# Kernel optimization log

Hardware: AMD Instinct MI355X
Metric: run time of the kernel (lower is better)

## Reference

```python
import jax, jax.numpy as jnp
import numpy as np

MARGIN = 0.2
PAIR_EPS = 1e-6   # torch pairwise_distance eps inside TripletMarginLoss
NORM_EPS = 1e-12  # F.normalize eps


def setup_inputs() -> dict:
    key = jax.random.key(0)
    k1, k2, k3 = jax.random.split(key, 3)
    bs, C, D = 64, 1024, 64
    inputs = jax.random.normal(k1, (bs, C, D), dtype=jnp.float32)
    label = jax.random.randint(k2, (bs, C, 1), 0, 2).astype(jnp.float32)
    prot = jax.random.normal(k3, (C, D), dtype=jnp.float32)
    prot = prot / jnp.linalg.norm(prot, axis=1, keepdims=True)
    return {"inputs": inputs, "label": label, "pos_prot": prot, "only_update": 0}


def reference(inputs, label, pos_prot, only_update):
    bs, C, D = inputs.shape
    # F.normalize(p=2, dim=1) per class slice == normalize over last dim of [bs,C,D]
    nrm = jnp.linalg.norm(inputs, axis=-1, keepdims=True)
    x = inputs / jnp.maximum(nrm, NORM_EPS)                      # [bs,C,D]

    # torch.cdist(x, prot): euclidean distances [bs, C(anchor cls), C(prot)]
    x2 = jnp.sum(x * x, axis=-1)                                 # [bs,C]
    p2 = jnp.sum(pos_prot * pos_prot, axis=-1)                   # [C]
    xp = jnp.einsum('bcd,kd->bck', x, pos_prot)                  # [bs,C,C]
    d2 = x2[:, :, None] + p2[None, None, :] - 2.0 * xp
    prot_dist = jnp.sqrt(jnp.maximum(d2, 0.0))                   # [bs,C,C]

    # hard negative: nearest prototype excluding the anchor's own class
    # (argsort + skip-self loop == masked argmin)
    eye = jnp.eye(C, dtype=bool)[None, :, :]
    neg_cls = jnp.argmin(jnp.where(eye, jnp.inf, prot_dist), axis=-1)  # [bs,C]

    positives = pos_prot[None, :, :]                             # [1,C,D] (broadcast of repeat)
    negatives = pos_prot[neg_cls]                                # [bs,C,D]

    # TripletMarginLoss(margin=0.2, p=2, reduction='none'), eps inside distance
    d_ap = jnp.linalg.norm(x - positives + PAIR_EPS, axis=-1)    # [bs,C]
    d_an = jnp.linalg.norm(x - negatives + PAIR_EPS, axis=-1)    # [bs,C]
    tri = jnp.maximum(d_ap - d_an + MARGIN, 0.0)                 # [bs,C]

    w = label[:, :, 0]                                           # [bs,C]
    loss = jnp.mean(jnp.sum(tri * w, axis=-1) / jnp.sum(w, axis=-1))
    return loss
```

## Files before the change

kernel.cpp:

```cpp
#include <hip/hip_runtime.h>
#include <cfloat>

#define BS 64
#define C  1024
#define D  64
#define CT 128
#define NX8 (BS * C * D / 8)

typedef __attribute__((ext_vector_type(8))) short short8;
typedef __attribute__((ext_vector_type(4))) float f32x4;
typedef unsigned short ushort_t;
typedef unsigned int uint_t;

__device__ __forceinline__ ushort_t f2bf(float f) {
    uint_t u = __float_as_uint(f);
    u += 0x7fffu + ((u >> 16) & 1u);
    return (ushort_t)(u >> 16);
}

__global__ __launch_bounds__(256)
void prep_cvt(const float* __restrict__ inputs, const float* __restrict__ prot,
              ushort_t* __restrict__ xhg, ushort_t* __restrict__ phg)
{
    const int idx = blockIdx.x * 256 + threadIdx.x;
    const bool isX = idx < NX8;
    const int rel = isX ? idx : idx - NX8;
    const float* sb = isX ? inputs : prot;
    ushort_t* db = isX ? xhg : phg;

    const int ft = rel >> 7, w = rel & 127, h = w >> 6, ln = w & 63;
    const int rr = ft * 16 + (ln & 15), dg = h * 4 + (ln >> 4);
    const float* s = sb + (size_t)rr * D + dg * 8;
    float4 a = *(const float4*)s;
    float4 b2 = *(const float4*)(s + 4);
    float x[8] = {a.x, a.y, a.z, a.w, b2.x, b2.y, b2.z, b2.w};
    short8 hv;
    #pragma unroll
    for (int e = 0; e < 8; e++) hv[e] = (short)f2bf(x[e]);
    ((short8*)db)[rel] = hv;
}

__global__ __launch_bounds__(512, 4)
void triplet_mfma(const float* __restrict__ inputs,
                  const float* __restrict__ label,
                  const float* __restrict__ prot,
                  const ushort_t* __restrict__ xhg,
                  const ushort_t* __restrict__ phg,
                  float* __restrict__ part)
{
    __shared__ short8 bsh[32 * 128];
    __shared__ uint_t redk[CT][4];
    __shared__ float  wred[16];

    const int tid  = threadIdx.x;
    const int lane = tid & 63;
    const int wid  = tid >> 6;
    const int wr   = wid >> 2;
    const int wc   = wid & 3;
    const int b    = blockIdx.x >> 3;
    const int c0   = (blockIdx.x & 7) * CT;

    const short8* BH = (const short8*)phg;
    const short8* XH = (const short8*)xhg;

    const size_t ftb = (size_t)blockIdx.x * 8 + wr * 4;
    short8 ah[4][2];
    #pragma unroll
    for (int i = 0; i < 4; i++) {
        ah[i][0] = XH[(ftb + i) * 128 + lane];
        ah[i][1] = XH[(ftb + i) * 128 + 64 + lane];
    }

    uint_t bestk[16];
    #pragma unroll
    for (int q = 0; q < 16; q++) bestk[q] = 0u;

    const uint_t MMASK = 0xFFFFFC00u;
    const int rowtile0 = (c0 >> 4) + wr * 4;
    const int rsub = (lane >> 4) * 4;
    const int csub = lane & 15;

    auto process = [&](int jg, short8 b0, short8 b1) {
        const uint_t cidx = (uint_t)(1023 - (jg * 16 + csub));
        #pragma unroll
        for (int i = 0; i < 4; i++) {
            f32x4 acc = {16.f, 16.f, 16.f, 16.f};
            acc = __builtin_amdgcn_mfma_f32_16x16x32_bf16(ah[i][0], b0, acc, 0, 0, 0);
            acc = __builtin_amdgcn_mfma_f32_16x16x32_bf16(ah[i][1], b1, acc, 0, 0, 0);
            const bool dtile = (rowtile0 + i) == jg;
            #pragma unroll
            for (int r = 0; r < 4; r++) {
                uint_t key = (__float_as_uint(acc[r]) & MMASK) | cidx;
                if (dtile && (rsub + r) == csub) key = 0u;
                bestk[i * 4 + r] = bestk[i * 4 + r] > key ? bestk[i * 4 + r] : key;
            }
        }
    };

    for (int ch = 0; ch < 2; ch++) {
        if (ch) __syncthreads();
        const short8* src = BH + (size_t)ch * 4096;
        #pragma unroll
        for (int it = 0; it < 8; it++)
            bsh[it * 512 + tid] = src[it * 512 + tid];
        __syncthreads();

        const int base = wc * 8;
        short8 cb0 = bsh[(base + 0) * 128 + lane];
        short8 cb1 = bsh[(base + 0) * 128 + 64 + lane];
        #pragma unroll
        for (int lt = 0; lt < 8; lt++) {
            const int nt = (lt + 1 < 8) ? lt + 1 : 7;
            short8 n0 = bsh[(base + nt) * 128 + lane];
            short8 n1 = bsh[(base + nt) * 128 + 64 + lane];
            __builtin_amdgcn_sched_barrier(0);
            process(ch * 32 + base + lt, cb0, cb1);
            cb0 = n0; cb1 = n1;
        }
    }

    #pragma unroll
    for (int i = 0; i < 4; i++)
        #pragma unroll
        for (int r = 0; r < 4; r++) {
            uint_t v = bestk[i * 4 + r];
            #pragma unroll
            for (int off = 1; off < 16; off <<= 1) {
                uint_t ov = (uint_t)__shfl_xor((int)v, off);
                v = v > ov ? v : ov;
            }
            if (csub == 0) redk[wr * 64 + i * 16 + rsub + r][wc] = v;
        }
    __syncthreads();

    float num = 0.f, den = 0.f;
    {
        const int row = tid >> 2, p4 = tid & 3;
        uint_t kk = redk[row][p4];
        {
            uint_t o1 = (uint_t)__shfl_xor((int)kk, 1); kk = kk > o1 ? kk : o1;
            uint_t o2 = (uint_t)__shfl_xor((int)kk, 2); kk = kk > o2 ? kk : o2;
        }
        const int bi = 1023 - (int)(kk & 0x3FFu);
        const int cg = c0 + row;

        const float4* xr = (const float4*)(inputs + (size_t)(b * C + cg) * D) + p4 * 4;
        float4 xv[4];
        float x2 = 0.f;
        #pragma unroll
        for (int q = 0; q < 4; q++) {
            xv[q] = xr[q];
            x2 = fmaf(xv[q].x, xv[q].x, fmaf(xv[q].y, xv[q].y,
                 fmaf(xv[q].z, xv[q].z, fmaf(xv[q].w, xv[q].w, x2))));
        }
        x2 += __shfl_xor(x2, 1);
        x2 += __shfl_xor(x2, 2);
        const float inv = 1.0f / fmaxf(sqrtf(x2), 1e-12f);

        const float4* pp = (const float4*)(prot + (size_t)cg * D) + p4 * 4;
        const float4* pn = (const float4*)(prot + (size_t)bi * D) + p4 * 4;
        float sap = 0.f, san = 0.f;
        #pragma unroll
        for (int q = 0; q < 4; q++) {
            float4 aa = pp[q];
            float4 nn = pn[q];
            float t;
            t = fmaf(xv[q].x, inv, -aa.x) + 1e-6f;  sap = fmaf(t, t, sap);
            t = fmaf(xv[q].y, inv, -aa.y) + 1e-6f;  sap = fmaf(t, t, sap);
            t = fmaf(xv[q].z, inv, -aa.z) + 1e-6f;  sap = fmaf(t, t, sap);
            t = fmaf(xv[q].w, inv, -aa.w) + 1e-6f;  sap = fmaf(t, t, sap);
            t = fmaf(xv[q].x, inv, -nn.x) + 1e-6f;  san = fmaf(t, t, san);
            t = fmaf(xv[q].y, inv, -nn.y) + 1e-6f;  san = fmaf(t, t, san);
            t = fmaf(xv[q].z, inv, -nn.z) + 1e-6f;  san = fmaf(t, t, san);
            t = fmaf(xv[q].w, inv, -nn.w) + 1e-6f;  san = fmaf(t, t, san);
        }
        sap += __shfl_xor(sap, 1);  sap += __shfl_xor(sap, 2);
        san += __shfl_xor(san, 1);  san += __shfl_xor(san, 2);
        if (p4 == 0) {
            float tri = fmaxf(sqrtf(sap) - sqrtf(san) + 0.2f, 0.0f);
            float w   = label[b * C + cg];
            num = tri * w;
            den = w;
        }
    }

    #pragma unroll
    for (int off = 1; off < 64; off <<= 1) {
        num += __shfl_xor(num, off);
        den += __shfl_xor(den, off);
    }
    if (lane == 0) { wred[wid * 2] = num; wred[wid * 2 + 1] = den; }
    __syncthreads();

    if (tid == 0) {
        float sn = 0.f, sd = 0.f;
        #pragma unroll
        for (int wv = 0; wv < 8; wv++) { sn += wred[wv * 2]; sd += wred[wv * 2 + 1]; }
        part[blockIdx.x * 2 + 0] = sn;
        part[blockIdx.x * 2 + 1] = sd;
    }
}

__global__ void triplet_finish(const float* __restrict__ part, float* __restrict__ out)
{
    int t = threadIdx.x;
    float num = 0.f, den = 0.f;
    #pragma unroll
    for (int h = 0; h < 8; h++) {
        num += part[(t * 8 + h) * 2 + 0];
        den += part[(t * 8 + h) * 2 + 1];
    }
    float v = num / den;
    #pragma unroll
    for (int off = 32; off > 0; off >>= 1) v += __shfl_down(v, off);
    if (t == 0) out[0] = v * (1.0f / (float)BS);
}

extern "C" void kernel_launch(void* const* d_in, const int* in_sizes, int n_in,
                              void* d_out, int out_size, void* d_ws, size_t ws_size,
                              hipStream_t stream)
{
    const float* inputs = (const float*)d_in[0];
    const float* label  = (const float*)d_in[1];
    const float* prot   = (const float*)d_in[2];
    float* out = (float*)d_out;

    ushort_t* xhg  = (ushort_t*)d_ws;
    ushort_t* phg  = xhg + (size_t)BS * C * D;
    float*    part = (float*)(phg + (size_t)C * D);

    prep_cvt<<<dim3((NX8 + C * D / 8) / 256), dim3(256), 0, stream>>>(
        inputs, prot, xhg, phg);
    triplet_mfma<<<dim3(BS * (C / CT)), dim3(512), 0, stream>>>(
        inputs, label, prot, xhg, phg, part);
    triplet_finish<<<1, 64, 0, stream>>>(part, out);
}
```

Before: 28.04 us.

## Fuse input bf16 conversion into main MFMA kernel, prep only prototypes

Removes the separate pass that converted the whole inputs tensor to bf16 in a workspace. Each block of the main kernel now loads its own 128x64 input tile, converts it to bf16 into LDS, and reads its MFMA A-fragments from there. A small kernel still converts the prototypes into the MFMA-friendly layout. This avoids writing and re-reading a 8MB bf16 copy of the inputs, at the cost of extra conversion work and two barriers inside the main kernel.

```diff
diff --git a/kernel.cpp b/kernel.cpp
--- a/kernel.cpp
+++ b/kernel.cpp
@@ -5,7 +5,6 @@
 #define C  1024
 #define D  64
 #define CT 128
-#define NX8 (BS * C * D / 8)
 
 typedef __attribute__((ext_vector_type(8))) short short8;
 typedef __attribute__((ext_vector_type(4))) float f32x4;
@@ -18,33 +17,29 @@
     return (ushort_t)(u >> 16);
 }
 
-__global__ __launch_bounds__(256)
-void prep_cvt(const float* __restrict__ inputs, const float* __restrict__ prot,
-              ushort_t* __restrict__ xhg, ushort_t* __restrict__ phg)
-{
-    const int idx = blockIdx.x * 256 + threadIdx.x;
-    const bool isX = idx < NX8;
-    const int rel = isX ? idx : idx - NX8;
-    const float* sb = isX ? inputs : prot;
-    ushort_t* db = isX ? xhg : phg;
-
-    const int ft = rel >> 7, w = rel & 127, h = w >> 6, ln = w & 63;
-    const int rr = ft * 16 + (ln & 15), dg = h * 4 + (ln >> 4);
-    const float* s = sb + (size_t)rr * D + dg * 8;
-    float4 a = *(const float4*)s;
-    float4 b2 = *(const float4*)(s + 4);
-    float x[8] = {a.x, a.y, a.z, a.w, b2.x, b2.y, b2.z, b2.w};
-    short8 hv;
-    #pragma unroll
-    for (int e = 0; e < 8; e++) hv[e] = (short)f2bf(x[e]);
-    ((short8*)db)[rel] = hv;
+__global__ void prep_prot(const float* __restrict__ prot, ushort_t* __restrict__ ph)
+{
+    const int k = blockIdx.x * 128 + threadIdx.x;
+    const float4* row = (const float4*)(prot + (size_t)k * D);
+    const int jt = k >> 4;
+    #pragma unroll
+    for (int dg = 0; dg < 8; dg++) {
+        float4 a = row[dg * 2];
+        float4 b = row[dg * 2 + 1];
+        float x[8] = {a.x, a.y, a.z, a.w, b.x, b.y, b.z, b.w};
+        short8 hv;
+        #pragma unroll
+        for (int e = 0; e < 8; e++) hv[e] = (short)f2bf(x[e]);
+        const int h  = dg >> 2;
+        const int ln = (k & 15) + (dg & 3) * 16;
+        ((short8*)ph)[(size_t)jt * 128 + h * 64 + ln] = hv;
+    }
 }
 
 __global__ __launch_bounds__(512, 4)
 void triplet_mfma(const float* __restrict__ inputs,
                   const float* __restrict__ label,
                   const float* __restrict__ prot,
-                  const ushort_t* __restrict__ xhg,
                   const ushort_t* __restrict__ phg,
                   float* __restrict__ part)
 {
@@ -61,15 +56,31 @@
     const int c0   = (blockIdx.x & 7) * CT;
 
     const short8* BH = (const short8*)phg;
-    const short8* XH = (const short8*)xhg;
-
-    const size_t ftb = (size_t)blockIdx.x * 8 + wr * 4;
+
+    #pragma unroll
+    for (int it = 0; it < 2; it++) {
+        const int rel = tid + it * 512;
+        const int ft = rel >> 7, w = rel & 127, h = w >> 6, ln = w & 63;
+        const int rr = ft * 16 + (ln & 15), dg = h * 4 + (ln >> 4);
+        const float* s = inputs + (size_t)(b * C + c0 + rr) * D + dg * 8;
+        float4 a  = *(const float4*)s;
+        float4 b2 = *(const float4*)(s + 4);
+        short8 hv;
+        hv[0] = (short)f2bf(a.x);  hv[1] = (short)f2bf(a.y);
+        hv[2] = (short)f2bf(a.z);  hv[3] = (short)f2bf(a.w);
+        hv[4] = (short)f2bf(b2.x); hv[5] = (short)f2bf(b2.y);
+        hv[6] = (short)f2bf(b2.z); hv[7] = (short)f2bf(b2.w);
+        bsh[rel] = hv;
+    }
+    __syncthreads();
+
     short8 ah[4][2];
     #pragma unroll
     for (int i = 0; i < 4; i++) {
-        ah[i][0] = XH[(ftb + i) * 128 + lane];
-        ah[i][1] = XH[(ftb + i) * 128 + 64 + lane];
-    }
+        ah[i][0] = bsh[(wr * 4 + i) * 128 + lane];
+        ah[i][1] = bsh[(wr * 4 + i) * 128 + 64 + lane];
+    }
+    __syncthreads();
 
     uint_t bestk[16];
     #pragma unroll
@@ -225,13 +236,11 @@
     const float* prot   = (const float*)d_in[2];
     float* out = (float*)d_out;
 
-    ushort_t* xhg  = (ushort_t*)d_ws;
-    ushort_t* phg  = xhg + (size_t)BS * C * D;
+    ushort_t* phg  = (ushort_t*)d_ws;
     float*    part = (float*)(phg + (size_t)C * D);
 
-    prep_cvt<<<dim3((NX8 + C * D / 8) / 256), dim3(256), 0, stream>>>(
-        inputs, prot, xhg, phg);
+    prep_prot<<<dim3(C / 128), dim3(128), 0, stream>>>(prot, phg);
     triplet_mfma<<<dim3(BS * (C / CT)), dim3(512), 0, stream>>>(
-        inputs, label, prot, xhg, phg, part);
+        inputs, label, prot, phg, part);
     triplet_finish<<<1, 64, 0, stream>>>(part, out);
 }
```

Result: faster. 27.35 us (-2.4%).
